# Kernel optimization log

Measured on AMD Instinct MI355X. Metric: run time of the kernel, lower is better.

Reference implementation:

```python
import jax, jax.numpy as jnp
import numpy as np


def _extract_patches(x, k):
    # tf.image.extract_patches(sizes=[1,k,k,1], strides=1, rates=1, padding='SAME')
    # reshaped to [B,H,W,k*k,C]; window ordered row-major (di, dj), zero padded.
    B, H, W, C = x.shape
    p = k // 2
    xp = jnp.pad(x, ((0, 0), (p, p), (p, p), (0, 0)))
    # fixed k*k=25 shifted views; stacking along new patch axis
    views = [xp[:, i:i + H, j:j + W, :] for i in range(k) for j in range(k)]
    return jnp.stack(views, axis=3)  # [B,H,W,k*k,C]


def reference(main, main_value, ref, ref_value, k_size=5):
    # main/ref: [B,H,W,C]; main_value/ref_value: [B,H,W,V]
    ref_p = _extract_patches(ref, k_size)            # [B,H,W,K,C], K=k*k
    refv_p = _extract_patches(ref_value, k_size)     # [B,H,W,K,V]

    # scores for the K neighbor slots plus one self slot (main concat at end)
    scores_nbr = jnp.einsum('bhwkc,bhwc->bhwk', ref_p, main)   # [B,H,W,K]
    score_self = jnp.einsum('bhwc,bhwc->bhw', main, main)      # [B,H,W]
    scores = jnp.concatenate([scores_nbr, score_self[..., None]], axis=-1)  # [B,H,W,K+1]

    attn = jax.nn.softmax(scores, axis=-1)                     # [B,H,W,K+1]

    values = jnp.concatenate([refv_p, main_value[:, :, :, None, :]], axis=3)  # [B,H,W,K+1,V]
    out = jnp.einsum('bhwk,bhwkv->bhwv', attn, values)         # [B,H,W,V]
    return out


def setup_inputs() -> dict:
    key = jax.random.key(0)
    k1, k2, k3, k4 = jax.random.split(key, 4)
    B, H, W, C, V = 2, 128, 128, 256, 64
    return {
        'main': jax.random.normal(k1, (B, H, W, C), dtype=jnp.float32),
        'main_value': jax.random.normal(k2, (B, H, W, V), dtype=jnp.float32),
        'ref': jax.random.normal(k3, (B, H, W, C), dtype=jnp.float32),
        'ref_value': jax.random.normal(k4, (B, H, W, V), dtype=jnp.float32),
    }
```

## Files before the change

### kernel.cpp

```cpp
#include <hip/hip_runtime.h>
#include <math.h>

namespace {

constexpr int Bn = 2, Hn = 128, Wn = 128, Cn = 256, Vn = 64;

__device__ __forceinline__ void load8(float* r, const float* p) {
    float4 a = *(const float4*)(p);
    float4 b = *(const float4*)(p + 4);
    r[0]=a.x; r[1]=a.y; r[2]=a.z; r[3]=a.w;
    r[4]=b.x; r[5]=b.y; r[6]=b.z; r[7]=b.w;
}

template <int CTRL>
__device__ __forceinline__ float row_add(float v) {
    int sh = __builtin_amdgcn_update_dpp(0, __float_as_int(v), CTRL, 0xF, 0xF, true);
    return v + __int_as_float(sh);
}

__device__ __forceinline__ float split_reduce(float v) {
    v = row_add<0xB1>(v);
    v = row_add<0x4E>(v);
    v = row_add<0x124>(v);
    v = row_add<0x128>(v);
    v += __int_as_float(__builtin_amdgcn_ds_swizzle(__float_as_int(v), 0x401F));
    return v;
}

__global__ __launch_bounds__(256)
void local_attn_kernel(const float* __restrict__ mainp,
                       const float* __restrict__ mainv,
                       const float* __restrict__ refp,
                       const float* __restrict__ refv,
                       float* __restrict__ outp)
{
    const int t = threadIdx.x;
    const int s = t & 31;
    const int g = t >> 5;
    const int blk = blockIdx.x;
    const int seg = blk & 7;
    const int h   = (blk >> 3) & (Hn - 1);
    const int b   = blk >> 10;
    const int w0  = seg * 16 + g * 2;
    const int rowbase = b * Hn + h;

    float m0[8], m1[8];
    const float* mp = mainp + ((size_t)rowbase * Wn + w0) * Cn + s * 8;
    load8(m0, mp);
    load8(m1, mp + Cn);

    float self0 = 0.f, self1 = 0.f;
    #pragma unroll
    for (int c = 0; c < 8; ++c) {
        self0 = fmaf(m0[c], m0[c], self0);
        self1 = fmaf(m1[c], m1[c], self1);
    }
    self0 = split_reduce(self0);
    self1 = split_reduce(self1);

    float mx0 = self0, mx1 = self1, den0 = 1.f, den1 = 1.f;
    float acc0[2], acc1[2];
    {
        const float* mvp = mainv + ((size_t)rowbase * Wn + w0) * Vn + s * 2;
        float2 a = *(const float2*)(mvp);
        float2 c = *(const float2*)(mvp + Vn);
        acc0[0] = a.x; acc0[1] = a.y;
        acc1[0] = c.x; acc1[1] = c.y;
    }

    #pragma unroll 1
    for (int di = 0; di < 5; ++di) {
        const int hh = h + di - 2;
        const bool rowok = (unsigned)hh < (unsigned)Hn;
        const size_t rbase = (size_t)(b * Hn + (rowok ? hh : 0)) * Wn;
        const float* rp = refp + rbase * Cn + s * 8;

        float sc0[5], sc1[5];
        #pragma unroll
        for (int o = 0; o < 6; ++o) {
            const int col = w0 - 2 + o;
            const bool ok = rowok && (unsigned)col < (unsigned)Wn;
            float r[8];
            #pragma unroll
            for (int c = 0; c < 8; ++c) r[c] = 0.f;
            if (ok) load8(r, rp + (size_t)col * Cn);
            if (o < 5) {
                float a = 0.f;
                #pragma unroll
                for (int c = 0; c < 8; ++c) a = fmaf(m0[c], r[c], a);
                sc0[o] = a;
            }
            if (o >= 1) {
                float a = 0.f;
                #pragma unroll
                for (int c = 0; c < 8; ++c) a = fmaf(m1[c], r[c], a);
                sc1[o - 1] = a;
            }
        }

        const float* rvp = refv + rbase * Vn + s * 2;
        float2 rv[6];
        #pragma unroll
        for (int o = 0; o < 6; ++o) {
            const int col = w0 - 2 + o;
            rv[o] = make_float2(0.f, 0.f);
            if (rowok && (unsigned)col < (unsigned)Wn)
                rv[o] = *(const float2*)(rvp + (size_t)col * Vn);
        }

        #pragma unroll
        for (int k = 0; k < 5; ++k) {
            sc0[k] = split_reduce(sc0[k]);
            sc1[k] = split_reduce(sc1[k]);
        }

        const float rm0 = fmaxf(fmaxf(fmaxf(sc0[0], sc0[1]), fmaxf(sc0[2], sc0[3])), sc0[4]);
        const float rm1 = fmaxf(fmaxf(fmaxf(sc1[0], sc1[1]), fmaxf(sc1[2], sc1[3])), sc1[4]);
        const float nm0 = fmaxf(mx0, rm0), nm1 = fmaxf(mx1, rm1);
        const float e0 = __expf(mx0 - nm0), e1 = __expf(mx1 - nm1);
        float sum0 = 0.f, sum1 = 0.f;
        #pragma unroll
        for (int k = 0; k < 5; ++k) {
            sc0[k] = __expf(sc0[k] - nm0); sum0 += sc0[k];
            sc1[k] = __expf(sc1[k] - nm1); sum1 += sc1[k];
        }
        den0 = den0 * e0 + sum0;
        den1 = den1 * e1 + sum1;
        acc0[0] *= e0; acc0[1] *= e0;
        acc1[0] *= e1; acc1[1] *= e1;
        mx0 = nm0; mx1 = nm1;

        #pragma unroll
        for (int o = 0; o < 6; ++o) {
            if (o < 5) {
                const float wkj = sc0[o];
                acc0[0] = fmaf(wkj, rv[o].x, acc0[0]);
                acc0[1] = fmaf(wkj, rv[o].y, acc0[1]);
            }
            if (o >= 1) {
                const float wkj = sc1[o - 1];
                acc1[0] = fmaf(wkj, rv[o].x, acc1[0]);
                acc1[1] = fmaf(wkj, rv[o].y, acc1[1]);
            }
        }
    }

    const float inv0 = 1.f / den0, inv1 = 1.f / den1;
    float* op = outp + ((size_t)rowbase * Wn + w0) * Vn + s * 2;
    float2 o0, o1;
    o0.x = acc0[0] * inv0; o0.y = acc0[1] * inv0;
    o1.x = acc1[0] * inv1; o1.y = acc1[1] * inv1;
    *(float2*)(op)      = o0;
    *(float2*)(op + Vn) = o1;
}

}

extern "C" void kernel_launch(void* const* d_in, const int* in_sizes, int n_in,
                              void* d_out, int out_size, void* d_ws, size_t ws_size,
                              hipStream_t stream)
{
    const float* mainp = (const float*)d_in[0];
    const float* mainv = (const float*)d_in[1];
    const float* refp  = (const float*)d_in[2];
    const float* refv  = (const float*)d_in[3];
    float* outp = (float*)d_out;

    dim3 grid(Bn * Hn * 8);
    dim3 block(256);
    hipLaunchKernelGGL(local_attn_kernel, grid, block, 0, stream,
                       mainp, mainv, refp, refv, outp);
}
```

Measured before the change: 35.36 us.

## Split local attention into parallel score kernel and softmax-aggregate kernel

Splits the single fused kernel in two. The first kernel computes the 25 neighbour dot products plus the self score, with one block per (row offset, row segment), which gives five times as many blocks. It writes them to a workspace buffer. The second kernel reads the scores per pixel, does the softmax, and accumulates the value vectors with float4 loads. This aims to raise parallelism and hide the latency of the serial per-row loop, at the cost of an extra launch, a workspace round-trip, and reloading main five times. It falls back to the old kernel if the workspace is too small.

Measured after the change: 69.12 us. 95.5% more time.

```diff
diff --git a/kernel.cpp b/kernel.cpp
--- a/kernel.cpp
+++ b/kernel.cpp
@@ -4,6 +4,8 @@
 namespace {
 
 constexpr int Bn = 2, Hn = 128, Wn = 128, Cn = 256, Vn = 64;
+constexpr int WSTR = 28;
+constexpr size_t WS_NEED = (size_t)Bn * Hn * Wn * WSTR * 4;
 
 __device__ __forceinline__ void load8(float* r, const float* p) {
     float4 a = *(const float4*)(p);
@@ -27,12 +29,162 @@
     return v;
 }
 
+__device__ __forceinline__ int clampi(int v, int lo, int hi) {
+    return v < lo ? lo : (v > hi ? hi : v);
+}
+
 __global__ __launch_bounds__(256)
-void local_attn_kernel(const float* __restrict__ mainp,
-                       const float* __restrict__ mainv,
-                       const float* __restrict__ refp,
-                       const float* __restrict__ refv,
-                       float* __restrict__ outp)
+void score_kernel(const float* __restrict__ mainp,
+                  const float* __restrict__ refp,
+                  float* __restrict__ wts)
+{
+    const int t = threadIdx.x;
+    const int s = t & 31;
+    const int g = t >> 5;
+    const int bid = blockIdx.x;
+    const int di  = bid >> 11;
+    const int blk = bid & 2047;
+    const int seg = blk & 7;
+    const int h   = (blk >> 3) & (Hn - 1);
+    const int b   = blk >> 10;
+    const int w0  = seg * 16 + g * 2;
+    const int rowbase = b * Hn + h;
+
+    float m0[8], m1[8];
+    const float* mp = mainp + ((size_t)rowbase * Wn + w0) * Cn + s * 8;
+    load8(m0, mp);
+    load8(m1, mp + Cn);
+
+    const int hh = h + di - 2;
+    const bool rowok = (unsigned)hh < (unsigned)Hn;
+    const size_t rbase = (size_t)(b * Hn + (rowok ? hh : 0)) * Wn;
+    const float* rp = refp + rbase * Cn + s * 8;
+
+    float sc0[5], sc1[5];
+    #pragma unroll
+    for (int o = 0; o < 6; ++o) {
+        const int col = w0 - 2 + o;
+        const bool ok = rowok && (unsigned)col < (unsigned)Wn;
+        float r[8];
+        #pragma unroll
+        for (int c = 0; c < 8; ++c) r[c] = 0.f;
+        if (ok) load8(r, rp + (size_t)col * Cn);
+        if (o < 5) {
+            float a = 0.f;
+            #pragma unroll
+            for (int c = 0; c < 8; ++c) a = fmaf(m0[c], r[c], a);
+            sc0[o] = a;
+        }
+        if (o >= 1) {
+            float a = 0.f;
+            #pragma unroll
+            for (int c = 0; c < 8; ++c) a = fmaf(m1[c], r[c], a);
+            sc1[o - 1] = a;
+        }
+    }
+
+    #pragma unroll
+    for (int k = 0; k < 5; ++k) {
+        sc0[k] = split_reduce(sc0[k]);
+        sc1[k] = split_reduce(sc1[k]);
+    }
+
+    float self0 = 0.f, self1 = 0.f;
+    if (di == 2) {
+        #pragma unroll
+        for (int c = 0; c < 8; ++c) {
+            self0 = fmaf(m0[c], m0[c], self0);
+            self1 = fmaf(m1[c], m1[c], self1);
+        }
+        self0 = split_reduce(self0);
+        self1 = split_reduce(self1);
+    }
+
+    float* p0 = wts + ((size_t)rowbase * Wn + w0) * WSTR + di * 5;
+    float* p1 = p0 + WSTR;
+    if (s == 0)  p0[0] = sc0[0];
+    if (s == 1)  p0[1] = sc0[1];
+    if (s == 2)  p0[2] = sc0[2];
+    if (s == 3)  p0[3] = sc0[3];
+    if (s == 4)  p0[4] = sc0[4];
+    if (s == 8)  p1[0] = sc1[0];
+    if (s == 9)  p1[1] = sc1[1];
+    if (s == 10) p1[2] = sc1[2];
+    if (s == 11) p1[3] = sc1[3];
+    if (s == 12) p1[4] = sc1[4];
+    if (di == 2) {
+        float* q = wts + ((size_t)rowbase * Wn + w0) * WSTR;
+        if (s == 16) q[25] = self0;
+        if (s == 24) q[WSTR + 25] = self1;
+    }
+}
+
+__global__ __launch_bounds__(256)
+void finish_kernel(const float* __restrict__ mainv,
+                   const float* __restrict__ refv,
+                   const float* __restrict__ wts,
+                   float* __restrict__ outp)
+{
+    const int t  = threadIdx.x;
+    const int s4 = t & 15;
+    const int p  = t >> 4;
+    const int blk = blockIdx.x;
+    const int seg = blk & 7;
+    const int h   = (blk >> 3) & (Hn - 1);
+    const int b   = blk >> 10;
+    const int w   = seg * 16 + p;
+    const int rowbase = b * Hn + h;
+    const size_t px = (size_t)rowbase * Wn + w;
+
+    const float* sp = wts + px * WSTR;
+    float wk[26];
+    #pragma unroll
+    for (int k = 0; k < 26; ++k) wk[k] = sp[k];
+
+    float mx = wk[25];
+    #pragma unroll
+    for (int k = 0; k < 25; ++k) mx = fmaxf(mx, wk[k]);
+    float den = 0.f;
+    #pragma unroll
+    for (int k = 0; k < 26; ++k) { wk[k] = __expf(wk[k] - mx); den += wk[k]; }
+
+    #pragma unroll
+    for (int k = 0; k < 25; ++k) {
+        const int di = k / 5, d = k % 5;
+        const bool ok = ((unsigned)(h + di - 2) < (unsigned)Hn) &&
+                        ((unsigned)(w + d  - 2) < (unsigned)Wn);
+        wk[k] = ok ? wk[k] : 0.f;
+    }
+
+    float acc[4];
+    {
+        float4 mv = *(const float4*)(mainv + px * Vn + s4 * 4);
+        acc[0] = wk[25] * mv.x; acc[1] = wk[25] * mv.y;
+        acc[2] = wk[25] * mv.z; acc[3] = wk[25] * mv.w;
+    }
+    #pragma unroll
+    for (int k = 0; k < 25; ++k) {
+        const int di = k / 5, d = k % 5;
+        const int rowc = clampi(h + di - 2, 0, Hn - 1);
+        const int colc = clampi(w + d  - 2, 0, Wn - 1);
+        const float4 rv = *(const float4*)(refv +
+            ((size_t)(b * Hn + rowc) * Wn + colc) * Vn + s4 * 4);
+        acc[0] = fmaf(wk[k], rv.x, acc[0]);
+        acc[1] = fmaf(wk[k], rv.y, acc[1]);
+        acc[2] = fmaf(wk[k], rv.z, acc[2]);
+        acc[3] = fmaf(wk[k], rv.w, acc[3]);
+    }
+
+    const float inv = 1.f / den;
+    float4 o;
+    o.x = acc[0] * inv; o.y = acc[1] * inv; o.z = acc[2] * inv; o.w = acc[3] * inv;
+    *(float4*)(outp + px * Vn + s4 * 4) = o;
+}
+
+__global__ __launch_bounds__(256)
+void fallback_kernel(const float* __restrict__ mainp, const float* __restrict__ mainv,
+                     const float* __restrict__ refp, const float* __restrict__ refv,
+                     float* __restrict__ outp)
 {
     const int t = threadIdx.x;
     const int s = t & 31;
@@ -97,7 +249,6 @@
                 sc1[o - 1] = a;
             }
         }
-
         const float* rvp = refv + rbase * Vn + s * 2;
         float2 rv[6];
         #pragma unroll
@@ -107,13 +258,11 @@
             if (rowok && (unsigned)col < (unsigned)Wn)
                 rv[o] = *(const float2*)(rvp + (size_t)col * Vn);
         }
-
         #pragma unroll
         for (int k = 0; k < 5; ++k) {
             sc0[k] = split_reduce(sc0[k]);
             sc1[k] = split_reduce(sc1[k]);
         }
-
         const float rm0 = fmaxf(fmaxf(fmaxf(sc0[0], sc0[1]), fmaxf(sc0[2], sc0[3])), sc0[4]);
         const float rm1 = fmaxf(fmaxf(fmaxf(sc1[0], sc1[1]), fmaxf(sc1[2], sc1[3])), sc1[4]);
         const float nm0 = fmaxf(mx0, rm0), nm1 = fmaxf(mx1, rm1);
@@ -129,7 +278,6 @@
         acc0[0] *= e0; acc0[1] *= e0;
         acc1[0] *= e1; acc1[1] *= e1;
         mx0 = nm0; mx1 = nm1;
-
         #pragma unroll
         for (int o = 0; o < 6; ++o) {
             if (o < 5) {
@@ -166,8 +314,15 @@
     const float* refv  = (const float*)d_in[3];
     float* outp = (float*)d_out;
 
-    dim3 grid(Bn * Hn * 8);
-    dim3 block(256);
-    hipLaunchKernelGGL(local_attn_kernel, grid, block, 0, stream,
-                       mainp, mainv, refp, refv, outp);
-}
+    if (ws_size < WS_NEED) {
+        hipLaunchKernelGGL(fallback_kernel, dim3(Bn * Hn * 8), dim3(256), 0, stream,
+                           mainp, mainv, refp, refv, outp);
+        return;
+    }
+
+    float* wts = (float*)d_ws;
+    hipLaunchKernelGGL(score_kernel, dim3(5 * Bn * Hn * 8), dim3(256), 0, stream,
+                       mainp, refp, wts);
+    hipLaunchKernelGGL(finish_kernel, dim3(Bn * Hn * 8), dim3(256), 0, stream,
+                       mainv, refv, wts, outp);
+}
```
